# Optimization experiments

Measured on AMD Instinct MI355X. Metric: run time of the kernel, lower is better.

## Reference

```python
import jax, jax.numpy as jnp
import numpy as np

N_NODES = 100000
N_EDGES = 1600000
IN_DIM = 128
HID = 64
OUT = 1


def setup_inputs() -> dict:
    key = jax.random.key(0)
    ks = jax.random.split(key, 8)
    x = jax.random.normal(ks[0], (N_NODES, IN_DIM), dtype=jnp.float32)
    edge_src = jax.random.randint(ks[1], (N_EDGES,), 0, N_NODES)
    edge_dst = jax.random.randint(ks[2], (N_EDGES,), 0, N_NODES)
    edge_weight = jax.random.uniform(ks[3], (N_EDGES,), dtype=jnp.float32)
    W1 = jax.random.normal(ks[4], (IN_DIM, HID), dtype=jnp.float32) / np.sqrt(IN_DIM)
    b1 = jnp.zeros((HID,), dtype=jnp.float32)
    W2 = jax.random.normal(ks[5], (HID, OUT), dtype=jnp.float32) / np.sqrt(HID)
    b2 = jnp.zeros((OUT,), dtype=jnp.float32)
    return {"x": x, "edge_src": edge_src, "edge_dst": edge_dst,
            "edge_weight": edge_weight, "W1": W1, "b1": b1, "W2": W2, "b2": b2}


def _spmm(edge_src, edge_dst, edge_weight, h):
    # adj_norm @ h: gather source rows, scale by edge weight, scatter-add to dst
    msgs = edge_weight[:, None] * h[edge_src]           # [E, D]
    return jax.ops.segment_sum(msgs, edge_dst, num_segments=N_NODES)


def reference(x, edge_src, edge_dst, edge_weight, W1, b1, W2, b2):
    # Layer 1: Linear -> SpMM -> relu (dropout is identity in eval mode)
    h = x @ W1 + b1                                      # [N, HID]
    h = _spmm(edge_src, edge_dst, edge_weight, h)
    h = jax.nn.relu(h)
    # Layer 2: Linear -> SpMM (no activation on final layer)
    h = h @ W2 + b2                                      # [N, OUT]
    h = _spmm(edge_src, edge_dst, edge_weight, h)
    return h
```

## Files before the change

### kernel.cpp

```cpp
#include <hip/hip_runtime.h>

#define IN_DIM 128
#define HID 64
#define SHIFT 8
#define BNODES 256
#define NBMAX 1024
#define CH 4096
#define SRCMASK 0xFFFFF
#define LDSCAP 6144
#define XSTR 130

using bf16x8 = __attribute__((ext_vector_type(8))) short;
using f32x4  = __attribute__((ext_vector_type(4))) float;

__device__ inline unsigned short f2bf(float f) {
  unsigned u = __float_as_uint(f);
  u += 0x7FFF + ((u >> 16) & 1);
  return (unsigned short)(u >> 16);
}
__device__ inline float bf2f_lo(unsigned v) {
  return __uint_as_float(v << 16);
}
__device__ inline float bf2f_hi(unsigned v) {
  return __uint_as_float(v & 0xFFFF0000u);
}

__device__ inline int xcd_chunk(int bid, int nch) {
  int q = nch >> 3, r = nch & 7;
  int xcd = bid & 7, idx = bid >> 3;
  return (xcd < r) ? xcd * (q + 1) + idx : r * (q + 1) + (xcd - r) * q + idx;
}

__global__ __launch_bounds__(256) void w1pack_kernel(
    const float* __restrict__ W1, unsigned short* __restrict__ W1b,
    int* __restrict__ bucket_size, int NB) {
  if (blockIdx.x == 0) {
    for (int i = threadIdx.x; i < NB; i += 256) bucket_size[i] = 0;
  }
  int idx = blockIdx.x * 256 + threadIdx.x;
  if (idx >= 4 * 4 * 64 * 8) return;
  int i    = idx & 7;
  int lane = (idx >> 3) & 63;
  int kc   = (idx >> 9) & 3;
  int jt   = idx >> 11;
  int k = kc * 32 + ((lane >> 4) << 3) + i;
  int n = jt * 16 + (lane & 15);
  W1b[idx] = f2bf(W1[k * HID + n]);
}

__global__ __launch_bounds__(256) void gemm1_kernel(
    const float* __restrict__ x, const unsigned short* __restrict__ W1b,
    const float* __restrict__ b1, unsigned short* __restrict__ h1, int N) {
  __shared__ unsigned short Xs[4][16][XSTR];
  const int lane = threadIdx.x & 63;
  const int w    = threadIdx.x >> 6;
  const int rblk = blockIdx.x * 64;

  for (int it = 0; it < 8; ++it) {
    int flat = it * 64 + lane;
    int row  = flat >> 5;
    int c4   = (flat & 31) * 4;
    int gr = rblk + w * 16 + row;
    if (gr > N - 1) gr = N - 1;
    float4 v = *reinterpret_cast<const float4*>(x + (long)gr * IN_DIM + c4);
    ushort4 o;
    o.x = f2bf(v.x); o.y = f2bf(v.y); o.z = f2bf(v.z); o.w = f2bf(v.w);
    *reinterpret_cast<ushort4*>(&Xs[w][row][c4]) = o;
  }
  __syncthreads();

  bf16x8 a[4];
#pragma unroll
  for (int kc = 0; kc < 4; ++kc) {
    a[kc] = *reinterpret_cast<const bf16x8*>(
        &Xs[w][lane & 15][kc * 32 + ((lane >> 4) << 3)]);
  }

  const uint4* wb = reinterpret_cast<const uint4*>(W1b);
#pragma unroll
  for (int jt = 0; jt < 4; ++jt) {
    f32x4 acc = {0.f, 0.f, 0.f, 0.f};
#pragma unroll
    for (int kc = 0; kc < 4; ++kc) {
      union { uint4 q; bf16x8 v; } bu;
      bu.q = wb[(jt * 4 + kc) * 64 + lane];
      acc = __builtin_amdgcn_mfma_f32_16x16x32_bf16(a[kc], bu.v, acc, 0, 0, 0);
    }
    const int col = jt * 16 + (lane & 15);
    const float bb = b1[col];
#pragma unroll
    for (int r = 0; r < 4; ++r) {
      int row = (lane >> 4) * 4 + r;
      int gr = rblk + w * 16 + row;
      if (gr < N) h1[(long)gr * HID + col] = f2bf(acc[r] + bb);
    }
  }
}

__global__ __launch_bounds__(256) void bucket_count_kernel(
    const int* __restrict__ dst, int* __restrict__ bucket_size,
    int* __restrict__ blockRel, int NB, int E, int NCH) {
  __shared__ int hist[NBMAX];
  const int c = xcd_chunk(blockIdx.x, NCH);
  for (int i = threadIdx.x; i < NB; i += 256) hist[i] = 0;
  __syncthreads();
  int base = c * CH;
  int end = min(base + CH, E);
  for (int k = base + threadIdx.x; k < end; k += 256)
    atomicAdd(&hist[dst[k] >> SHIFT], 1);
  __syncthreads();
  for (int i = threadIdx.x; i < NB; i += 256) {
    int cv = hist[i];
    int r = cv ? atomicAdd(&bucket_size[i], cv) : 0;
    blockRel[(long)c * NB + i] = r;
  }
}

__global__ __launch_bounds__(1024) void bucket_scan_kernel(
    const int* __restrict__ bucket_size, int* __restrict__ bucket_offs, int NB) {
  __shared__ int tmp[1024];
  int tid = threadIdx.x;
  int v = (tid < NB) ? bucket_size[tid] : 0;
  tmp[tid] = v;
  __syncthreads();
  for (int off = 1; off < 1024; off <<= 1) {
    int t = (tid >= off) ? tmp[tid - off] : 0;
    __syncthreads();
    tmp[tid] += t;
    __syncthreads();
  }
  if (tid <= NB) bucket_offs[tid] = tmp[tid] - v;
}

__global__ __launch_bounds__(256) void bucket_place_kernel(
    const int* __restrict__ src, const int* __restrict__ dst,
    const float* __restrict__ w, const int* __restrict__ bucket_offs,
    const int* __restrict__ blockRel, int2* __restrict__ bpart,
    int NB, int E, int NCH) {
  __shared__ int cur[NBMAX];
  const int c = xcd_chunk(blockIdx.x, NCH);
  for (int i = threadIdx.x; i < NB; i += 256)
    cur[i] = bucket_offs[i] + blockRel[(long)c * NB + i];
  __syncthreads();
  int base = c * CH;
  int end = min(base + CH, E);
  for (int k = base + threadIdx.x; k < end; k += 256) {
    int d = dst[k];
    int b = d >> SHIFT;
    int pos = atomicAdd(&cur[b], 1);
    bpart[pos] = make_int2((src[k] & SRCMASK) | ((d & (BNODES - 1)) << 20),
                           __float_as_int(w[k]));
  }
}

__global__ __launch_bounds__(256) void csr_place_kernel(
    const int2* __restrict__ bpart, const int* __restrict__ bucket_offs,
    int2* __restrict__ csr, int* __restrict__ noffs, int N, int NB, int E) {
  __shared__ int cnt[BNODES];
  __shared__ int cur[BNODES];
  __shared__ int wtot[4];
  __shared__ int2 ebuf[LDSCAP];
  const int t = threadIdx.x;
  const int b = blockIdx.x;
  const int beg = bucket_offs[b], end = bucket_offs[b + 1];
  const int len = end - beg;
  const bool useLds = (len <= LDSCAP);

  cnt[t] = 0;
  __syncthreads();

  if (useLds) {
    for (int k = t; k < len; k += 256) {
      int2 e = bpart[beg + k];
      ebuf[k] = e;
      atomicAdd(&cnt[e.x >> 20], 1);
    }
  } else {
    for (int k = beg + t; k < end; k += 256)
      atomicAdd(&cnt[bpart[k].x >> 20], 1);
  }
  __syncthreads();

  int v = cnt[t], s = v;
#pragma unroll
  for (int d = 1; d < 64; d <<= 1) {
    int u = __shfl_up(s, d, 64);
    if ((t & 63) >= d) s += u;
  }
  if ((t & 63) == 63) wtot[t >> 6] = s;
  __syncthreads();
  int base = 0;
  const int wv_ = t >> 6;
  if (wv_ > 0) base += wtot[0];
  if (wv_ > 1) base += wtot[1];
  if (wv_ > 2) base += wtot[2];
  const int g = beg + base + s - v;
  cur[t] = g;
  const int node = (b << SHIFT) + t;
  if (node < N) noffs[node] = g;
  if (b == NB - 1 && t == 0) noffs[N] = E;
  __syncthreads();

  if (useLds) {
    for (int k = t; k < len; k += 256) {
      int2 e = ebuf[k];
      int pos = atomicAdd(&cur[e.x >> 20], 1);
      csr[pos] = make_int2(e.x & SRCMASK, e.y);
    }
  } else {
    for (int k = beg + t; k < end; k += 256) {
      int2 e = bpart[k];
      int pos = atomicAdd(&cur[e.x >> 20], 1);
      csr[pos] = make_int2(e.x & SRCMASK, e.y);
    }
  }
}

__global__ __launch_bounds__(256) void spmm1_fused_kernel(
    const int* __restrict__ noffs, const int2* __restrict__ csr,
    const unsigned short* __restrict__ h1, const float* __restrict__ W2,
    const float* __restrict__ b2, float* __restrict__ h3, int N) {
  int wave = (blockIdx.x * 256 + threadIdx.x) >> 6;
  int lane = threadIdx.x & 63;
  if (wave >= N) return;
  int beg = noffs[wave], end = noffs[wave + 1];
  const int e8 = lane >> 3;
  const int l8 = lane & 7;

  float a0 = 0.f, a1 = 0.f, a2 = 0.f, a3 = 0.f;
  float a4 = 0.f, a5 = 0.f, a6 = 0.f, a7 = 0.f;
  int k = beg + e8;

  int2 eA, eB;
  if (k + 8 < end) { eA = csr[k]; eB = csr[k + 8]; }
  while (k + 8 < end) {
    uint4 vA = *reinterpret_cast<const uint4*>(h1 + (long)eA.x * HID + 8 * l8);
    uint4 vB = *reinterpret_cast<const uint4*>(h1 + (long)eB.x * HID + 8 * l8);
    float wA = __int_as_float(eA.y), wB = __int_as_float(eB.y);
    int kn = k + 16;
    if (kn + 8 < end) { eA = csr[kn]; eB = csr[kn + 8]; }
    a0 += wA * bf2f_lo(vA.x); a1 += wA * bf2f_hi(vA.x);
    a2 += wA * bf2f_lo(vA.y); a3 += wA * bf2f_hi(vA.y);
    a4 += wA * bf2f_lo(vA.z); a5 += wA * bf2f_hi(vA.z);
    a6 += wA * bf2f_lo(vA.w); a7 += wA * bf2f_hi(vA.w);
    a0 += wB * bf2f_lo(vB.x); a1 += wB * bf2f_hi(vB.x);
    a2 += wB * bf2f_lo(vB.y); a3 += wB * bf2f_hi(vB.y);
    a4 += wB * bf2f_lo(vB.z); a5 += wB * bf2f_hi(vB.z);
    a6 += wB * bf2f_lo(vB.w); a7 += wB * bf2f_hi(vB.w);
    k = kn;
  }
  for (; k < end; k += 8) {
    int2 e = csr[k];
    uint4 v = *reinterpret_cast<const uint4*>(h1 + (long)e.x * HID + 8 * l8);
    float w = __int_as_float(e.y);
    a0 += w * bf2f_lo(v.x); a1 += w * bf2f_hi(v.x);
    a2 += w * bf2f_lo(v.y); a3 += w * bf2f_hi(v.y);
    a4 += w * bf2f_lo(v.z); a5 += w * bf2f_hi(v.z);
    a6 += w * bf2f_lo(v.w); a7 += w * bf2f_hi(v.w);
  }

  {
    const bool hi = (e8 & 1);
    float s0 = hi ? a0 : a4;  float r0 = __shfl_xor(s0, 8, 64);
    float s1 = hi ? a1 : a5;  float r1 = __shfl_xor(s1, 8, 64);
    float s2 = hi ? a2 : a6;  float r2 = __shfl_xor(s2, 8, 64);
    float s3 = hi ? a3 : a7;  float r3 = __shfl_xor(s3, 8, 64);
    a0 = (hi ? a4 : a0) + r0;
    a1 = (hi ? a5 : a1) + r1;
    a2 = (hi ? a6 : a2) + r2;
    a3 = (hi ? a7 : a3) + r3;
  }
  {
    const bool hi = (e8 >> 1) & 1;
    float s0 = hi ? a0 : a2;  float r0 = __shfl_xor(s0, 16, 64);
    float s1 = hi ? a1 : a3;  float r1 = __shfl_xor(s1, 16, 64);
    a0 = (hi ? a2 : a0) + r0;
    a1 = (hi ? a3 : a1) + r1;
  }
  {
    const bool hi = (e8 >> 2) & 1;
    float s0 = hi ? a0 : a1;  float r0 = __shfl_xor(s0, 32, 64);
    a0 = (hi ? a1 : a0) + r0;
  }
  const int dim = 8 * l8 + 4 * (e8 & 1) + 2 * ((e8 >> 1) & 1) + ((e8 >> 2) & 1);
  float s = fmaxf(a0, 0.f) * W2[dim];
  s += __shfl_xor(s, 1, 64);
  s += __shfl_xor(s, 2, 64);
  s += __shfl_xor(s, 4, 64);
  s += __shfl_xor(s, 8, 64);
  s += __shfl_xor(s, 16, 64);
  s += __shfl_xor(s, 32, 64);
  if (lane == 0) h3[wave] = s + b2[0];
}

__global__ __launch_bounds__(256) void spmm2_gather_kernel(
    const int* __restrict__ noffs, const int2* __restrict__ csr,
    const float* __restrict__ h3, float* __restrict__ out, int N) {
  int n = blockIdx.x * 256 + threadIdx.x;
  if (n >= N) return;
  int beg = noffs[n], end = noffs[n + 1];
  float acc = 0.f;
  int k = beg;
  if (k < end && (k & 1)) {
    int2 e = csr[k];
    acc += __int_as_float(e.y) * h3[e.x];
    ++k;
  }
  for (; k + 1 < end; k += 2) {
    int4 e2 = *reinterpret_cast<const int4*>(&csr[k]);
    acc += __int_as_float(e2.y) * h3[e2.x];
    acc += __int_as_float(e2.w) * h3[e2.z];
  }
  if (k < end) {
    int2 e = csr[k];
    acc += __int_as_float(e.y) * h3[e.x];
  }
  out[n] = acc;
}

extern "C" void kernel_launch(void* const* d_in, const int* in_sizes, int n_in,
                              void* d_out, int out_size, void* d_ws, size_t ws_size,
                              hipStream_t stream) {
  const float* x    = (const float*)d_in[0];
  const int*   esrc = (const int*)d_in[1];
  const int*   edst = (const int*)d_in[2];
  const float* ew   = (const float*)d_in[3];
  const float* W1   = (const float*)d_in[4];
  const float* b1   = (const float*)d_in[5];
  const float* W2   = (const float*)d_in[6];
  const float* b2   = (const float*)d_in[7];
  float* out = (float*)d_out;

  const int N = in_sizes[0] / IN_DIM;
  const int E = in_sizes[1];
  const int NB = (N + BNODES - 1) >> SHIFT;
  const int NCH = (E + CH - 1) / CH;

  char* p = (char*)d_ws;
  auto alloc = [&](size_t bytes) {
    char* r = p;
    p += (bytes + 15) & ~(size_t)15;
    return r;
  };
  unsigned short* h1 = (unsigned short*)alloc((size_t)N * HID * sizeof(unsigned short));
  unsigned short* W1b= (unsigned short*)alloc((size_t)8192 * sizeof(unsigned short));
  float* h3          = (float*)alloc((size_t)N * sizeof(float));
  int*   bucket_size = (int*)alloc((size_t)NB * sizeof(int));
  int*   bucket_offs = (int*)alloc((size_t)(NB + 1) * sizeof(int));
  int*   noffs       = (int*)alloc((size_t)(N + 1) * sizeof(int));
  int*   blockRel    = (int*)alloc((size_t)NCH * NB * sizeof(int));
  int2*  bpart       = (int2*)alloc((size_t)E * sizeof(int2));
  int2*  csr         = (int2*)alloc((size_t)E * sizeof(int2));

  w1pack_kernel<<<32, 256, 0, stream>>>(W1, W1b, bucket_size, NB);
  gemm1_kernel<<<(N + 63) / 64, 256, 0, stream>>>(x, W1b, b1, h1, N);

  bucket_count_kernel<<<NCH, 256, 0, stream>>>(edst, bucket_size, blockRel, NB, E, NCH);
  bucket_scan_kernel<<<1, 1024, 0, stream>>>(bucket_size, bucket_offs, NB);
  bucket_place_kernel<<<NCH, 256, 0, stream>>>(esrc, edst, ew, bucket_offs,
                                               blockRel, bpart, NB, E, NCH);
  csr_place_kernel<<<NB, 256, 0, stream>>>(bpart, bucket_offs, csr, noffs, N, NB, E);

  spmm1_fused_kernel<<<(unsigned)(((long)N * 64 + 255) / 256), 256, 0, stream>>>(
      noffs, csr, h1, W2, b2, h3, N);

  spmm2_gather_kernel<<<(N + 255) / 256, 256, 0, stream>>>(noffs, csr, h3, out, N);
}
```

Before: 126.4 us.

## Fuse W1 packing into GEMM, vectorize edge loads, pack SpMM accumulators

Result: no change. 126.3 us (-0.1%).

```diff
diff --git a/kernel.cpp b/kernel.cpp
--- a/kernel.cpp
+++ b/kernel.cpp
@@ -12,6 +12,7 @@
 
 using bf16x8 = __attribute__((ext_vector_type(8))) short;
 using f32x4  = __attribute__((ext_vector_type(4))) float;
+using f32x2  = __attribute__((ext_vector_type(2))) float;
 
 __device__ inline unsigned short f2bf(float f) {
   unsigned u = __float_as_uint(f);
@@ -24,6 +25,9 @@
 __device__ inline float bf2f_hi(unsigned v) {
   return __uint_as_float(v & 0xFFFF0000u);
 }
+__device__ inline f32x2 unpk2(unsigned v) {
+  return (f32x2){bf2f_lo(v), bf2f_hi(v)};
+}
 
 __device__ inline int xcd_chunk(int bid, int nch) {
   int q = nch >> 3, r = nch & 7;
@@ -31,30 +35,29 @@
   return (xcd < r) ? xcd * (q + 1) + idx : r * (q + 1) + (xcd - r) * q + idx;
 }
 
-__global__ __launch_bounds__(256) void w1pack_kernel(
-    const float* __restrict__ W1, unsigned short* __restrict__ W1b,
+__global__ __launch_bounds__(256) void gemm1_kernel(
+    const float* __restrict__ x, const float* __restrict__ W1,
+    const float* __restrict__ b1, unsigned short* __restrict__ h1, int N,
     int* __restrict__ bucket_size, int NB) {
-  if (blockIdx.x == 0) {
-    for (int i = threadIdx.x; i < NB; i += 256) bucket_size[i] = 0;
-  }
-  int idx = blockIdx.x * 256 + threadIdx.x;
-  if (idx >= 4 * 4 * 64 * 8) return;
-  int i    = idx & 7;
-  int lane = (idx >> 3) & 63;
-  int kc   = (idx >> 9) & 3;
-  int jt   = idx >> 11;
-  int k = kc * 32 + ((lane >> 4) << 3) + i;
-  int n = jt * 16 + (lane & 15);
-  W1b[idx] = f2bf(W1[k * HID + n]);
-}
-
-__global__ __launch_bounds__(256) void gemm1_kernel(
-    const float* __restrict__ x, const unsigned short* __restrict__ W1b,
-    const float* __restrict__ b1, unsigned short* __restrict__ h1, int N) {
   __shared__ unsigned short Xs[4][16][XSTR];
+  __shared__ unsigned short Wb[8192];
   const int lane = threadIdx.x & 63;
   const int w    = threadIdx.x >> 6;
   const int rblk = blockIdx.x * 64;
+
+  if (blockIdx.x == 0) {
+    for (int i = threadIdx.x; i < NB; i += 256) bucket_size[i] = 0;
+  }
+
+  for (int idx = threadIdx.x; idx < 8192; idx += 256) {
+    int i  = idx & 7;
+    int ln = (idx >> 3) & 63;
+    int kc = (idx >> 9) & 3;
+    int jt = idx >> 11;
+    int k = kc * 32 + ((ln >> 4) << 3) + i;
+    int n = jt * 16 + (ln & 15);
+    Wb[idx] = f2bf(W1[k * HID + n]);
+  }
 
   for (int it = 0; it < 8; ++it) {
     int flat = it * 64 + lane;
@@ -76,7 +79,7 @@
         &Xs[w][lane & 15][kc * 32 + ((lane >> 4) << 3)]);
   }
 
-  const uint4* wb = reinterpret_cast<const uint4*>(W1b);
+  const uint4* wb = reinterpret_cast<const uint4*>(Wb);
 #pragma unroll
   for (int jt = 0; jt < 4; ++jt) {
     f32x4 acc = {0.f, 0.f, 0.f, 0.f};
@@ -106,7 +109,15 @@
   __syncthreads();
   int base = c * CH;
   int end = min(base + CH, E);
-  for (int k = base + threadIdx.x; k < end; k += 256)
+  for (int k = base + threadIdx.x * 4; k + 3 < end; k += 1024) {
+    int4 d4 = *reinterpret_cast<const int4*>(&dst[k]);
+    atomicAdd(&hist[d4.x >> SHIFT], 1);
+    atomicAdd(&hist[d4.y >> SHIFT], 1);
+    atomicAdd(&hist[d4.z >> SHIFT], 1);
+    atomicAdd(&hist[d4.w >> SHIFT], 1);
+  }
+  int tail_start = base + ((end - base) & ~3);
+  for (int k = tail_start + threadIdx.x; k < end; k += 256)
     atomicAdd(&hist[dst[k] >> SHIFT], 1);
   __syncthreads();
   for (int i = threadIdx.x; i < NB; i += 256) {
@@ -144,7 +155,25 @@
   __syncthreads();
   int base = c * CH;
   int end = min(base + CH, E);
-  for (int k = base + threadIdx.x; k < end; k += 256) {
+  for (int k = base + threadIdx.x * 4; k + 3 < end; k += 1024) {
+    int4   s4 = *reinterpret_cast<const int4*>(&src[k]);
+    int4   d4 = *reinterpret_cast<const int4*>(&dst[k]);
+    float4 w4 = *reinterpret_cast<const float4*>(&w[k]);
+    int p0 = atomicAdd(&cur[d4.x >> SHIFT], 1);
+    int p1 = atomicAdd(&cur[d4.y >> SHIFT], 1);
+    int p2 = atomicAdd(&cur[d4.z >> SHIFT], 1);
+    int p3 = atomicAdd(&cur[d4.w >> SHIFT], 1);
+    bpart[p0] = make_int2((s4.x & SRCMASK) | ((d4.x & (BNODES - 1)) << 20),
+                          __float_as_int(w4.x));
+    bpart[p1] = make_int2((s4.y & SRCMASK) | ((d4.y & (BNODES - 1)) << 20),
+                          __float_as_int(w4.y));
+    bpart[p2] = make_int2((s4.z & SRCMASK) | ((d4.z & (BNODES - 1)) << 20),
+                          __float_as_int(w4.z));
+    bpart[p3] = make_int2((s4.w & SRCMASK) | ((d4.w & (BNODES - 1)) << 20),
+                          __float_as_int(w4.w));
+  }
+  int tail_start = base + ((end - base) & ~3);
+  for (int k = tail_start + threadIdx.x; k < end; k += 256) {
     int d = dst[k];
     int b = d >> SHIFT;
     int pos = atomicAdd(&cur[b], 1);
@@ -227,8 +256,8 @@
   const int e8 = lane >> 3;
   const int l8 = lane & 7;
 
-  float a0 = 0.f, a1 = 0.f, a2 = 0.f, a3 = 0.f;
-  float a4 = 0.f, a5 = 0.f, a6 = 0.f, a7 = 0.f;
+  f32x2 a01 = {0.f, 0.f}, a23 = {0.f, 0.f};
+  f32x2 a45 = {0.f, 0.f}, a67 = {0.f, 0.f};
   int k = beg + e8;
 
   int2 eA, eB;
@@ -239,25 +268,30 @@
     float wA = __int_as_float(eA.y), wB = __int_as_float(eB.y);
     int kn = k + 16;
     if (kn + 8 < end) { eA = csr[kn]; eB = csr[kn + 8]; }
-    a0 += wA * bf2f_lo(vA.x); a1 += wA * bf2f_hi(vA.x);
-    a2 += wA * bf2f_lo(vA.y); a3 += wA * bf2f_hi(vA.y);
-    a4 += wA * bf2f_lo(vA.z); a5 += wA * bf2f_hi(vA.z);
-    a6 += wA * bf2f_lo(vA.w); a7 += wA * bf2f_hi(vA.w);
-    a0 += wB * bf2f_lo(vB.x); a1 += wB * bf2f_hi(vB.x);
-    a2 += wB * bf2f_lo(vB.y); a3 += wB * bf2f_hi(vB.y);
-    a4 += wB * bf2f_lo(vB.z); a5 += wB * bf2f_hi(vB.z);
-    a6 += wB * bf2f_lo(vB.w); a7 += wB * bf2f_hi(vB.w);
+    f32x2 wA2 = {wA, wA}, wB2 = {wB, wB};
+    a01 += wA2 * unpk2(vA.x);
+    a23 += wA2 * unpk2(vA.y);
+    a45 += wA2 * unpk2(vA.z);
+    a67 += wA2 * unpk2(vA.w);
+    a01 += wB2 * unpk2(vB.x);
+    a23 += wB2 * unpk2(vB.y);
+    a45 += wB2 * unpk2(vB.z);
+    a67 += wB2 * unpk2(vB.w);
     k = kn;
   }
   for (; k < end; k += 8) {
     int2 e = csr[k];
     uint4 v = *reinterpret_cast<const uint4*>(h1 + (long)e.x * HID + 8 * l8);
     float w = __int_as_float(e.y);
-    a0 += w * bf2f_lo(v.x); a1 += w * bf2f_hi(v.x);
-    a2 += w * bf2f_lo(v.y); a3 += w * bf2f_hi(v.y);
-    a4 += w * bf2f_lo(v.z); a5 += w * bf2f_hi(v.z);
-    a6 += w * bf2f_lo(v.w); a7 += w * bf2f_hi(v.w);
-  }
+    f32x2 w2v = {w, w};
+    a01 += w2v * unpk2(v.x);
+    a23 += w2v * unpk2(v.y);
+    a45 += w2v * unpk2(v.z);
+    a67 += w2v * unpk2(v.w);
+  }
+
+  float a0 = a01[0], a1 = a01[1], a2 = a23[0], a3 = a23[1];
+  float a4 = a45[0], a5 = a45[1], a6 = a67[0], a7 = a67[1];
 
   {
     const bool hi = (e8 & 1);
@@ -343,7 +377,6 @@
     return r;
   };
   unsigned short* h1 = (unsigned short*)alloc((size_t)N * HID * sizeof(unsigned short));
-  unsigned short* W1b= (unsigned short*)alloc((size_t)8192 * sizeof(unsigned short));
   float* h3          = (float*)alloc((size_t)N * sizeof(float));
   int*   bucket_size = (int*)alloc((size_t)NB * sizeof(int));
   int*   bucket_offs = (int*)alloc((size_t)(NB + 1) * sizeof(int));
@@ -352,8 +385,8 @@
   int2*  bpart       = (int2*)alloc((size_t)E * sizeof(int2));
   int2*  csr         = (int2*)alloc((size_t)E * sizeof(int2));
 
-  w1pack_kernel<<<32, 256, 0, stream>>>(W1, W1b, bucket_size, NB);
-  gemm1_kernel<<<(N + 63) / 64, 256, 0, stream>>>(x, W1b, b1, h1, N);
+  gemm1_kernel<<<(N + 63) / 64, 256, 0, stream>>>(x, W1, b1, h1, N,
+                                                  bucket_size, NB);
 
   bucket_count_kernel<<<NCH, 256, 0, stream>>>(edst, bucket_size, blockRel, NB, E, NCH);
   bucket_scan_kernel<<<1, 1024, 0, stream>>>(bucket_size, bucket_offs, NB);
```
